# Kernel tuning notes

Hardware: AMD Instinct MI355X
Metric: run time of the kernel (lower is better)

## Reference

```python
import jax, jax.numpy as jnp
import numpy as np

N = 5000          # nodes (pool_ratios = [2000/5000, 0.5])
KS = (2000, 1000, 500)  # top-k sizes per level, depth=3
H = 128           # inter_dim
IN = 3            # xyz
OUT = 6890        # SMPL template vertices
E = 80000


def _gcn(adj, x, W, b):
    # GCNConv: add self-loops (weight 1), symmetric normalization
    n = adj.shape[0]
    A = adj + jnp.eye(n, dtype=adj.dtype)
    dinv = jax.lax.rsqrt(A.sum(axis=1))
    Ahat = dinv[:, None] * A * dinv[None, :]
    return Ahat @ (x @ W) + b


def _augment(adj):
    # GraphUNet.augment_adj: remove self loops, add self loops, A @ A, remove self loops
    n = adj.shape[0]
    eye = jnp.eye(n, dtype=adj.dtype)
    A = adj * (1.0 - eye) + eye
    A2 = A @ A
    return A2 * (1.0 - eye)


def _pool(x, adj, w, k):
    # TopKPooling: score = tanh(x.w / ||w||), keep top-k, scale kept features by score
    score = jnp.tanh((x @ w) / jnp.linalg.norm(w))
    sc, perm = jax.lax.top_k(score, k)
    x = x[perm] * sc[:, None]
    adj = adj[perm][:, perm]
    return x, adj, perm


def reference(pos, edge_index, Wd0, bd0, Wd1, bd1, Wd2, bd2, Wd3, bd3,
              pw0, pw1, pw2, Wu0, bu0, Wu1, bu1, Wu2, bu2,
              W1, b1, W2, b2, W3, b3):
    # eval mode: dropout_adj(p=0.1, training=False) is identity
    adj = jnp.zeros((N, N), pos.dtype).at[edge_index[0], edge_index[1]].add(1.0)

    x = jax.nn.relu(_gcn(adj, pos, Wd0, bd0))
    xs, adjs, perms = [x], [adj], []
    Wds = [(Wd1, bd1), (Wd2, bd2), (Wd3, bd3)]
    pws = [pw0, pw1, pw2]

    adj_cur = adj
    for i in range(3):
        a = _augment(adj_cur)
        x, adj_cur, perm = _pool(x, a, pws[i], KS[i])
        Wi, bi = Wds[i]
        x = jax.nn.relu(_gcn(adj_cur, x, Wi, bi))
        if i < 2:
            xs.append(x)
            adjs.append(adj_cur)
        perms.append(perm)

    Wus = [(Wu0, bu0), (Wu1, bu1), (Wu2, bu2)]
    for i in range(3):
        j = 2 - i
        res = xs[j]
        up = jnp.zeros_like(res).at[perms[j]].set(x)  # unpool: scatter back
        x = res + up                                   # sum_res=True
        Wi, bi = Wus[i]
        x = _gcn(adjs[j], x, Wi, bi)
        if i < 2:
            x = jax.nn.relu(x)

    x = x @ W1 + b1
    x = jax.nn.relu(x) @ W2 + b2
    x = x @ W3 + b3
    return jax.nn.log_softmax(x, axis=1)


def _glorot(k, shape):
    return (jax.random.normal(k, shape) * np.sqrt(2.0 / (shape[0] + shape[1]))).astype(jnp.float32)


def setup_inputs() -> dict:
    key = jax.random.key(0)
    ks = jax.random.split(key, 16)
    inp = {
        'pos': jax.random.normal(ks[0], (N, IN), dtype=jnp.float32),
        'edge_index': jax.random.randint(ks[1], (2, E), 0, N, dtype=jnp.int64),
        'Wd0': _glorot(ks[2], (IN, H)), 'bd0': jnp.zeros((H,), jnp.float32),
        'Wd1': _glorot(ks[3], (H, H)), 'bd1': jnp.zeros((H,), jnp.float32),
        'Wd2': _glorot(ks[4], (H, H)), 'bd2': jnp.zeros((H,), jnp.float32),
        'Wd3': _glorot(ks[5], (H, H)), 'bd3': jnp.zeros((H,), jnp.float32),
        'pw0': jax.random.normal(ks[6], (H,), dtype=jnp.float32) / np.sqrt(H),
        'pw1': jax.random.normal(ks[7], (H,), dtype=jnp.float32) / np.sqrt(H),
        'pw2': jax.random.normal(ks[8], (H,), dtype=jnp.float32) / np.sqrt(H),
        'Wu0': _glorot(ks[9], (H, H)), 'bu0': jnp.zeros((H,), jnp.float32),
        'Wu1': _glorot(ks[10], (H, H)), 'bu1': jnp.zeros((H,), jnp.float32),
        'Wu2': _glorot(ks[11], (H, H)), 'bu2': jnp.zeros((H,), jnp.float32),
        'W1': _glorot(ks[12], (H, H)), 'b1': jnp.zeros((H,), jnp.float32),
        'W2': _glorot(ks[13], (H, H)), 'b2': jnp.zeros((H,), jnp.float32),
        'W3': _glorot(ks[14], (H, OUT)), 'b3': jnp.zeros((OUT,), jnp.float32),
    }
    return inp
```

## Files before the change

### kernel.cpp

```cpp
#include <hip/hip_runtime.h>
#include <cmath>

#define CDIV(a,b) (((a)+(b)-1)/(b))

using u16 = unsigned short;
using short8 = __attribute__((ext_vector_type(8))) short;
using f32x4 = __attribute__((ext_vector_type(4))) float;

__device__ __forceinline__ u16 f2b(float v) {
    union { float f; unsigned u; } x; x.f = v;
    unsigned r = x.u + 0x7fffu + ((x.u >> 16) & 1u);
    return (u16)(r >> 16);
}
__device__ __forceinline__ float b2f(u16 h) {
    union { unsigned u; float f; } x; x.u = ((unsigned)h) << 16;
    return x.f;
}

#if defined(__has_builtin)
#if __has_builtin(__builtin_amdgcn_global_load_lds)
#define HAS_GLL 1
#endif
#endif
#ifndef HAS_GLL
#define HAS_GLL 0
#endif

__device__ __forceinline__ void g2l(const u16* g, uint4* l) {
#if HAS_GLL
    __builtin_amdgcn_global_load_lds((const __attribute__((address_space(1))) void*)g,
                                     (__attribute__((address_space(3))) void*)l, 16, 0, 0);
#else
    *l = *(const uint4*)g;
#endif
}


__global__ void build_adj_k(const int* __restrict__ ei, float* __restrict__ adj, int E, int ld) {
    int e = blockIdx.x * 256 + threadIdx.x;
    if (e < E) {
        int s = ei[e];
        int d = ei[E + e];
        atomicAdd(&adj[(size_t)s * ld + d], 1.0f);
    }
}

__global__ void rowsum_dinv_b_k(const u16* __restrict__ adjb, int ld, int n, float* __restrict__ dinv) {
    int i = blockIdx.x;
    __shared__ float red[256];
    const u16* row = adjb + (size_t)i * ld;
    float s = 0.f;
    for (int j = threadIdx.x; j < n; j += 256) s += b2f(row[j]);
    red[threadIdx.x] = s; __syncthreads();
    for (int w = 128; w > 0; w >>= 1) {
        if (threadIdx.x < w) red[threadIdx.x] += red[threadIdx.x + w];
        __syncthreads();
    }
    if (threadIdx.x == 0) dinv[i] = rsqrtf(red[0] + 1.0f);
}

__global__ void conv0_k(const float* __restrict__ in, u16* __restrict__ outS, u16* __restrict__ outT, int n) {
    __shared__ u16 t[64][65];
    int i0 = blockIdx.y * 64, j0 = blockIdx.x * 64;
    for (int e = threadIdx.x; e < 4096; e += 256) {
        int r = e >> 6, c = e & 63;
        u16 v = f2b(in[(size_t)(i0 + r) * n + j0 + c]);
        outS[(size_t)(i0 + r) * n + j0 + c] = v;
        t[r][c] = v;
    }
    __syncthreads();
    for (int e = threadIdx.x; e < 4096; e += 256) {
        int r = e >> 6, c = e & 63;
        outT[(size_t)(j0 + r) * n + i0 + c] = t[c][r];
    }
}

__global__ void transpose_b_k(const u16* __restrict__ in, u16* __restrict__ out, int n) {
    __shared__ u16 t[64][65];
    int i0 = blockIdx.y * 64, j0 = blockIdx.x * 64;
    for (int e = threadIdx.x; e < 4096; e += 256) {
        int r = e >> 6, c = e & 63;
        t[r][c] = in[(size_t)(i0 + r) * n + j0 + c];
    }
    __syncthreads();
    for (int e = threadIdx.x; e < 4096; e += 256) {
        int r = e >> 6, c = e & 63;
        out[(size_t)(j0 + r) * n + i0 + c] = t[c][r];
    }
}


template<int SA, int SB>
__global__ __launch_bounds__(256) void mm_nt(const u16* __restrict__ A0, const u16* __restrict__ A1,
                                             const u16* __restrict__ B0, const u16* __restrict__ B1,
                                             float* __restrict__ C, const float* __restrict__ cbias,
                                             int M, int N, int lda, int ldb, int ldc,
                                             int kPerZ, int Kpad, size_t cstride) {
    __shared__ uint4 lds_t[(2 + SA + SB) * 512];
    uint4* Ab  = lds_t;
    uint4* A1b = lds_t + (SA ? 512 : 0);
    uint4* Bb  = lds_t + (1 + SA) * 512;
    uint4* B1b = Bb + (SB ? 512 : 0);

    int tid = threadIdx.x;

    int nx = gridDim.x, nxy = nx * gridDim.y;
    int bx = blockIdx.x, by = blockIdx.y;
    if ((nxy & 7) == 0) {
        int flat = by * nx + bx;
        int nf = (flat & 7) * (nxy >> 3) + (flat >> 3);
        bx = nf % nx; by = nf / nx;
    }
    int row0 = by * 128, col0 = bx * 128;

    int kbeg = blockIdx.z * kPerZ;
    int kend = min(kbeg + kPerZ, Kpad);
    C += (size_t)blockIdx.z * cstride;

    int wave = tid >> 6, lane = tid & 63;
    int wr = (wave >> 1) * 64, wc = (wave & 1) * 64;
    int lrow = lane & 15, kg = lane >> 4;

    int tS0 = tid, tS1 = tid + 256;
    int R0 = ((tS0 >> 6) << 4) | (tS0 & 15), kc0 = (tS0 >> 4) & 3;
    int R1 = ((tS1 >> 6) << 4) | (tS1 & 15), kc1 = (tS1 >> 4) & 3;

    const u16* aP0 = A0 + (size_t)(row0 + R0) * lda + kbeg + kc0 * 8;
    const u16* aP1 = A0 + (size_t)(row0 + R1) * lda + kbeg + kc1 * 8;
    const u16* bP0 = B0 + (size_t)(col0 + R0) * ldb + kbeg + kc0 * 8;
    const u16* bP1 = B0 + (size_t)(col0 + R1) * ldb + kbeg + kc1 * 8;
    const u16* a1P0 = SA ? (A1 + (size_t)(row0 + R0) * lda + kbeg + kc0 * 8) : nullptr;
    const u16* a1P1 = SA ? (A1 + (size_t)(row0 + R1) * lda + kbeg + kc1 * 8) : nullptr;
    const u16* b1P0 = SB ? (B1 + (size_t)(col0 + R0) * ldb + kbeg + kc0 * 8) : nullptr;
    const u16* b1P1 = SB ? (B1 + (size_t)(col0 + R1) * ldb + kbeg + kc1 * 8) : nullptr;

    f32x4 acc[4][4] = {};

    for (int k0 = kbeg; k0 < kend; k0 += 32) {
        __syncthreads();
        g2l(aP0, Ab + tS0);
        g2l(aP1, Ab + tS1);
        if constexpr (SA) { g2l(a1P0, A1b + tS0); g2l(a1P1, A1b + tS1); }
        g2l(bP0, Bb + tS0);
        g2l(bP1, Bb + tS1);
        if constexpr (SB) { g2l(b1P0, B1b + tS0); g2l(b1P1, B1b + tS1); }
        __syncthreads();

        const short8* Ap  = (const short8*)Ab;
        const short8* A1p = (const short8*)A1b;
        const short8* Bp  = (const short8*)Bb;
        const short8* B1p = (const short8*)B1b;

        short8 a[4], a1[4], b[4], b1[4];
#pragma unroll
        for (int m = 0; m < 4; ++m) {
            int idx = (((wr >> 4) + m) << 6) | (kg << 4) | lrow;
            a[m] = Ap[idx];
            if constexpr (SA) a1[m] = A1p[idx];
        }
#pragma unroll
        for (int n = 0; n < 4; ++n) {
            int idx = (((wc >> 4) + n) << 6) | (kg << 4) | lrow;
            b[n] = Bp[idx];
            if constexpr (SB) b1[n] = B1p[idx];
        }
#pragma unroll
        for (int m = 0; m < 4; ++m)
#pragma unroll
            for (int n = 0; n < 4; ++n) {
                acc[m][n] = __builtin_amdgcn_mfma_f32_16x16x32_bf16(a[m], b[n], acc[m][n], 0, 0, 0);
                if constexpr (SA) acc[m][n] = __builtin_amdgcn_mfma_f32_16x16x32_bf16(a1[m], b[n], acc[m][n], 0, 0, 0);
                if constexpr (SB) acc[m][n] = __builtin_amdgcn_mfma_f32_16x16x32_bf16(a[m], b1[n], acc[m][n], 0, 0, 0);
            }

        aP0 += 32; aP1 += 32; bP0 += 32; bP1 += 32;
        if constexpr (SA) { a1P0 += 32; a1P1 += 32; }
        if constexpr (SB) { b1P0 += 32; b1P1 += 32; }
    }

#pragma unroll
    for (int m = 0; m < 4; ++m) {
        int rm = row0 + wr + m * 16 + kg * 4;
#pragma unroll
        for (int n = 0; n < 4; ++n) {
            int cc = col0 + wc + n * 16 + lrow;
            if (cc >= N) continue;
            float badd = cbias ? cbias[cc] : 0.f;
#pragma unroll
            for (int i = 0; i < 4; ++i) {
                int r = rm + i;
                if (r < M) C[(size_t)r * ldc + cc] = acc[m][n][i] + badd;
            }
        }
    }
}


__global__ __launch_bounds__(256) void gemm64(const float* __restrict__ A, const float* __restrict__ B,
                                              float* __restrict__ C,
                                              int M, int N, int K, int lda, int ldb, int ldc,
                                              const float* __restrict__ bias, int relu) {
    __shared__ float As[16][65];
    __shared__ float Bs[16][65];
    int tid = threadIdx.x;
    int trow = tid / 16, tcol = tid % 16;
    int row0 = blockIdx.y * 64 + trow * 4;
    int col0 = blockIdx.x * 64 + tcol * 4;
    float acc[4][4] = {};
    int am = tid >> 2;
    int ak = (tid & 3) * 4;
    int bk = tid >> 4;
    int bn = (tid & 15) * 4;
    for (int k0 = 0; k0 < K; k0 += 16) {
        int gm = blockIdx.y * 64 + am;
#pragma unroll
        for (int u = 0; u < 4; ++u) {
            int gk = k0 + ak + u;
            As[ak + u][am] = (gm < M && gk < K) ? A[(size_t)gm * lda + gk] : 0.f;
        }
        int gbk = k0 + bk;
#pragma unroll
        for (int u = 0; u < 4; ++u) {
            int gn = blockIdx.x * 64 + bn + u;
            Bs[bk][bn + u] = (gbk < K && gn < N) ? B[(size_t)gbk * ldb + gn] : 0.f;
        }
        __syncthreads();
#pragma unroll
        for (int kk = 0; kk < 16; ++kk) {
            float a[4], b[4];
#pragma unroll
            for (int i = 0; i < 4; ++i) a[i] = As[kk][trow * 4 + i];
#pragma unroll
            for (int j = 0; j < 4; ++j) b[j] = Bs[kk][tcol * 4 + j];
#pragma unroll
            for (int i = 0; i < 4; ++i)
#pragma unroll
                for (int j = 0; j < 4; ++j) acc[i][j] += a[i] * b[j];
        }
        __syncthreads();
    }
#pragma unroll
    for (int i = 0; i < 4; ++i) {
        int r = row0 + i;
        if (r >= M) continue;
#pragma unroll
        for (int j = 0; j < 4; ++j) {
            int c = col0 + j;
            if (c < N) {
                float v = acc[i][j] + (bias ? bias[c] : 0.f);
                if (relu) v = fmaxf(v, 0.f);
                C[(size_t)r * ldc + c] = v;
            }
        }
    }
}


__global__ void scale_split_k(const float* __restrict__ xw, const float* __restrict__ dinv,
                              u16* __restrict__ zhT, u16* __restrict__ zlT, int M, int ldz) {
    __shared__ float t[32][33];
    int i0 = blockIdx.x * 32, f0 = blockIdx.y * 32;
#pragma unroll
    for (int it = 0; it < 4; ++it) {
        int r = it * 8 + (threadIdx.x >> 5);
        int c = threadIdx.x & 31;
        int i = i0 + r;
        t[r][c] = (i < M) ? dinv[i] * xw[(size_t)i * 128 + f0 + c] : 0.f;
    }
    __syncthreads();
#pragma unroll
    for (int it = 0; it < 4; ++it) {
        int r = it * 8 + (threadIdx.x >> 5);
        int c = threadIdx.x & 31;
        int f = f0 + r, i = i0 + c;
        float v = t[c][r];
        u16 h = f2b(v);
        zhT[(size_t)f * ldz + i] = h;
        zlT[(size_t)f * ldz + i] = f2b(v - b2f(h));
    }
}

__global__ void reduce_gcn_post_k(const float* __restrict__ part, int Z, int Mp,
                                  const float* __restrict__ xw, const float* __restrict__ dinv,
                                  const float* __restrict__ bias, float* __restrict__ y, int relu) {
    int i = blockIdx.x, f = threadIdx.x;
    size_t idx = (size_t)i * 128 + f;
    float s = 0.f;
    for (int z = 0; z < Z; ++z) s += part[(size_t)z * Mp * 128 + idx];
    float di = dinv[i];
    float v = di * s + di * di * xw[idx] + bias[f];
    y[idx] = relu ? fmaxf(v, 0.f) : v;
}


__global__ void score_k(const float* __restrict__ x, const float* __restrict__ pw,
                        float* __restrict__ score) {
    int i = blockIdx.x;
    __shared__ float red[128], red2[128];
    float p = pw[threadIdx.x];
    red[threadIdx.x]  = x[(size_t)i * 128 + threadIdx.x] * p;
    red2[threadIdx.x] = p * p;
    __syncthreads();
    for (int s = 64; s > 0; s >>= 1) {
        if (threadIdx.x < s) { red[threadIdx.x] += red[threadIdx.x + s]; red2[threadIdx.x] += red2[threadIdx.x + s]; }
        __syncthreads();
    }
    if (threadIdx.x == 0) score[i] = tanhf(red[0] / sqrtf(red2[0]));
}

__global__ __launch_bounds__(256) void rank_partial_k(const float* __restrict__ score, int n,
                                                      int* __restrict__ rankpart) {
    __shared__ float s_sh[512];
    int i = blockIdx.x * 256 + threadIdx.x;
    int jbase = blockIdx.y * 512;
    float si = (i < n) ? score[i] : -3.0f;
    for (int t = threadIdx.x; t < 512; t += 256) {
        int j = jbase + t;
        s_sh[t] = (j < n) ? score[j] : -3.0f;
    }
    __syncthreads();
    int cnt = 0;
#pragma unroll 16
    for (int t = 0; t < 512; ++t) {
        float sj = s_sh[t];
        cnt += (sj > si) || (sj == si && (jbase + t) < i);
    }
    if (i < n) rankpart[blockIdx.y * n + i] = cnt;
}

__global__ void scatter_topk_k(const float* __restrict__ score, const int* __restrict__ rankpart,
                               int nsl, int n, int k, int* __restrict__ perm, float* __restrict__ sc) {
    int i = blockIdx.x * 256 + threadIdx.x;
    if (i >= n) return;
    int r = 0;
    for (int s = 0; s < nsl; ++s) r += rankpart[s * n + i];
    if (r < k) { perm[r] = i; sc[r] = score[i]; }
}

__global__ void pool_x_k(float* __restrict__ xo, const float* __restrict__ xi,
                         const int* __restrict__ perm, const float* __restrict__ sc) {
    int a = blockIdx.x, f = threadIdx.x;
    xo[(size_t)a * 128 + f] = xi[(size_t)perm[a] * 128 + f] * sc[a];
}

__global__ void gather2_b_k(const u16* __restrict__ src0, const u16* __restrict__ src1,
                            int ldsrc, const int* __restrict__ perm,
                            u16* __restrict__ dst0, u16* __restrict__ dst1, int width) {
    const u16* src = blockIdx.y ? src1 : src0;
    u16* dst = blockIdx.y ? dst1 : dst0;
    int row = blockIdx.x;
    int p = perm[row];
    const uint4* s4 = (const uint4*)(src + (size_t)p * ldsrc);
    uint4* d4 = (uint4*)(dst + (size_t)row * width);
    int n8 = width >> 3;
    for (int j = threadIdx.x; j < n8; j += 256) d4[j] = s4[j];
    __syncthreads();
    if (threadIdx.x == 0) dst[(size_t)row * width + p] = 0x3F80;
}

__global__ void reduce_pool_k(const float* __restrict__ part, int Z, int k, int Mp, u16* __restrict__ out) {
    int row = blockIdx.x;
    for (int j = threadIdx.x; j < Mp; j += 256) {
        float s = 0.f;
        if (row < k && j < k) {
            for (int z = 0; z < Z; ++z) s += part[(size_t)z * Mp * Mp + (size_t)row * Mp + j];
            if (j == row) s = 0.f;
        }
        out[(size_t)row * Mp + j] = f2b(s);
    }
}

__global__ void scatter_add_k(float* __restrict__ xdst, const int* __restrict__ perm,
                              const float* __restrict__ xsrc) {
    int a = blockIdx.x, f = threadIdx.x;
    xdst[(size_t)perm[a] * 128 + f] += xsrc[(size_t)a * 128 + f];
}


__global__ void split_head_k(const float* __restrict__ x, u16* __restrict__ Ah, u16* __restrict__ Al) {
    int i = blockIdx.x, f = threadIdx.x;
    size_t idx = (size_t)i * 128 + f;
    float v = x[idx];
    u16 h = f2b(v);
    Ah[idx] = h;
    Al[idx] = f2b(v - b2f(h));
}

__global__ void convW3T_k(const float* __restrict__ W3, u16* __restrict__ W3T, int Nc, int Ncp) {
    __shared__ float t[64][65];
    int k0 = blockIdx.y * 64, n0 = blockIdx.x * 64;
    for (int e = threadIdx.x; e < 4096; e += 256) {
        int r = e >> 6, c = e & 63;
        t[r][c] = (k0 + r < 128 && n0 + c < Nc) ? W3[(size_t)(k0 + r) * Nc + n0 + c] : 0.f;
    }
    __syncthreads();
    for (int e = threadIdx.x; e < 4096; e += 256) {
        int r = e >> 6, c = e & 63;
        int nn = n0 + r, kk = k0 + c;
        if (nn < Ncp) W3T[(size_t)nn * 128 + kk] = f2b(t[c][r]);
    }
}

__global__ __launch_bounds__(256) void logsoftmax_k(float* __restrict__ out) {
    const int C = 6890;
    const int CPT = 27;
    int row = blockIdx.x;
    float* rowp = out + (size_t)row * C;
    __shared__ float red[256];

    float v[CPT];
    float mx = -1e30f;
#pragma unroll
    for (int u = 0; u < CPT; ++u) {
        int c = threadIdx.x + u * 256;
        v[u] = (c < C) ? rowp[c] : -1e30f;
        mx = fmaxf(mx, v[u]);
    }
    red[threadIdx.x] = mx; __syncthreads();
    for (int s = 128; s > 0; s >>= 1) {
        if (threadIdx.x < s) red[threadIdx.x] = fmaxf(red[threadIdx.x], red[threadIdx.x + s]);
        __syncthreads();
    }
    float m = red[0];
    __syncthreads();

    float sum = 0.f;
#pragma unroll
    for (int u = 0; u < CPT; ++u) sum += __expf(v[u] - m);
    red[threadIdx.x] = sum; __syncthreads();
    for (int s = 128; s > 0; s >>= 1) {
        if (threadIdx.x < s) red[threadIdx.x] += red[threadIdx.x + s];
        __syncthreads();
    }
    float ls = m + logf(red[0]);

#pragma unroll
    for (int u = 0; u < CPT; ++u) {
        int c = threadIdx.x + u * 256;
        if (c < C) rowp[c] = v[u] - ls;
    }
}


extern "C" void kernel_launch(void* const* d_in, const int* in_sizes, int n_in,
                              void* d_out, int out_size, void* d_ws, size_t ws_size,
                              hipStream_t stream) {
    const int N0 = 5000, K1 = 2000, K2 = 1000, K3 = 500, E = 80000, OUTC = 6890;
    const int Np0 = 5120, Kp1 = 2048, Kp2 = 1024, Kp3 = 512, OUTCP = 6912;
    (void)in_sizes; (void)n_in; (void)out_size; (void)ws_size;

    const float* pos = (const float*)d_in[0];
    const int*   ei  = (const int*)d_in[1];
    const float* Wd0 = (const float*)d_in[2];  const float* bd0 = (const float*)d_in[3];
    const float* Wd1 = (const float*)d_in[4];  const float* bd1 = (const float*)d_in[5];
    const float* Wd2 = (const float*)d_in[6];  const float* bd2 = (const float*)d_in[7];
    const float* Wd3 = (const float*)d_in[8];  const float* bd3 = (const float*)d_in[9];
    const float* pw0 = (const float*)d_in[10];
    const float* pw1 = (const float*)d_in[11];
    const float* pw2 = (const float*)d_in[12];
    const float* Wu0 = (const float*)d_in[13]; const float* bu0 = (const float*)d_in[14];
    const float* Wu1 = (const float*)d_in[15]; const float* bu1 = (const float*)d_in[16];
    const float* Wu2 = (const float*)d_in[17]; const float* bu2 = (const float*)d_in[18];
    const float* W1  = (const float*)d_in[19]; const float* b1  = (const float*)d_in[20];
    const float* W2  = (const float*)d_in[21]; const float* b2  = (const float*)d_in[22];
    const float* W3  = (const float*)d_in[23]; const float* b3  = (const float*)d_in[24];

    float* w = (float*)d_ws;
    size_t off = 0;
    auto alloc = [&](size_t nel) { float* p = w + off; off += nel; return p; };

    float* pool = alloc(26220000);
    float* adj0 = pool;
    float* partials = pool;
    u16* G   = (u16*)(pool + 13000000);
    u16* HT  = (u16*)(pool + 18250000);
    u16* zhT = (u16*)(pool + 13000000);
    u16* zlT = (u16*)(pool + 13400000);
    u16* Ah  = (u16*)(pool);
    u16* Al  = (u16*)(pool + 400000);

    u16* adj0b  = (u16*)alloc(13107200);
    u16* adj0bT = (u16*)alloc(13107200);
    u16* adj1b  = (u16*)alloc(2097152);
    u16* adj1bT = (u16*)alloc(2097152);
    u16* adj2b  = (u16*)alloc(524288);
    u16* adj2bT = (u16*)alloc(524288);
    u16* adj3b  = (u16*)alloc(131072);
    u16* W3T    = (u16*)alloc(442368);

    float* x0 = alloc((size_t)N0 * 128);
    float* x1 = alloc((size_t)K1 * 128);
    float* x2 = alloc((size_t)K2 * 128);
    float* xa = alloc((size_t)N0 * 128);
    float* xb = alloc((size_t)N0 * 128);
    float* xw = alloc((size_t)N0 * 128);
    float* dinv0 = alloc(N0); float* dinv1 = alloc(K1); float* dinv2 = alloc(K2); float* dinv3 = alloc(K3);
    float* scorev = alloc(N0);
    float* scv    = alloc(K1);
    int* perm0 = (int*)alloc(K1);
    int* perm1 = (int*)alloc(K2);
    int* perm2 = (int*)alloc(K3);
    int* rankpart = (int*)alloc(50048);

    auto launch_mm = [&](int SA, int SB, const u16* A0, const u16* A1, const u16* B0, const u16* B1,
                         float* Cc, const float* cbias, int M, int N, int Kpad,
                         int lda, int ldb, int ldc, size_t cstride, int Z) -> int {
        int kPerZ = CDIV(Kpad, Z * 32) * 32;
        int gz = CDIV(Kpad, kPerZ);
        dim3 g(CDIV(N, 128), CDIV(M, 128), gz);
        if (SA)      mm_nt<1, 0><<<g, 256, 0, stream>>>(A0, A1, B0, B1, Cc, cbias, M, N, lda, ldb, ldc, kPerZ, Kpad, cstride);
        else if (SB) mm_nt<0, 1><<<g, 256, 0, stream>>>(A0, A1, B0, B1, Cc, cbias, M, N, lda, ldb, ldc, kPerZ, Kpad, cstride);
        else         mm_nt<0, 0><<<g, 256, 0, stream>>>(A0, A1, B0, B1, Cc, cbias, M, N, lda, ldb, ldc, kPerZ, Kpad, cstride);
        return gz;
    };

    auto run_gcn = [&](const u16* adjb, int n, int Np,
                       const float* x, int kin, const float* W, const float* bias,
                       const float* dinv, int relu, float* y, int Z) {
        gemm64<<<dim3(2, CDIV(n, 64)), 256, 0, stream>>>(x, W, xw, n, 128, kin, kin, 128, 128, nullptr, 0);
        scale_split_k<<<dim3(Np / 32, 4), 256, 0, stream>>>(xw, dinv, zhT, zlT, n, Np);
        int gz = launch_mm(0, 1, adjb, nullptr, zhT, zlT, partials, nullptr,
                           Np, 128, Np, Np, Np, 128, (size_t)Np * 128, Z);
        reduce_gcn_post_k<<<n, 128, 0, stream>>>(partials, gz, Np, xw, dinv, bias, y, relu);
    };

    auto run_pool = [&](const float* x, int n, int Np, int kNew, int KpNew, const float* pw,
                        const u16* srcb, const u16* srcbT, u16* adjNew, int* perm, int Z) {
        score_k<<<n, 128, 0, stream>>>(x, pw, scorev);
        int nsl = CDIV(n, 512);
        rank_partial_k<<<dim3(CDIV(n, 256), nsl), 256, 0, stream>>>(scorev, n, rankpart);
        scatter_topk_k<<<CDIV(n, 256), 256, 0, stream>>>(scorev, rankpart, nsl, n, kNew, perm, scv);
        pool_x_k<<<kNew, 128, 0, stream>>>(xa, x, perm, scv);
        gather2_b_k<<<dim3(kNew, 2), 256, 0, stream>>>(srcb, srcbT, Np, perm, G, HT, Np);
        int gz = launch_mm(0, 0, G, nullptr, HT, nullptr, partials, nullptr,
                           KpNew, KpNew, Np, Np, Np, KpNew, (size_t)KpNew * KpNew, Z);
        reduce_pool_k<<<KpNew, 256, 0, stream>>>(partials, gz, kNew, KpNew, adjNew);
    };

    hipMemsetAsync(adj0, 0, (size_t)Np0 * Np0 * sizeof(float), stream);
    build_adj_k<<<CDIV(E, 256), 256, 0, stream>>>(ei, adj0, E, Np0);
    conv0_k<<<dim3(Np0 / 64, Np0 / 64), 256, 0, stream>>>(adj0, adj0b, adj0bT, Np0);
    rowsum_dinv_b_k<<<N0, 256, 0, stream>>>(adj0b, Np0, Np0, dinv0);

    run_gcn(adj0b, N0, Np0, pos, 3, Wd0, bd0, dinv0, 1, x0, 10);

    run_pool(x0, N0, Np0, K1, Kp1, pw0, adj0b, adj0bT, adj1b, perm0, 3);
    transpose_b_k<<<dim3(Kp1 / 64, Kp1 / 64), 256, 0, stream>>>(adj1b, adj1bT, Kp1);
    rowsum_dinv_b_k<<<K1, 256, 0, stream>>>(adj1b, Kp1, Kp1, dinv1);
    run_gcn(adj1b, K1, Kp1, xa, 128, Wd1, bd1, dinv1, 1, x1, 16);

    run_pool(x1, K1, Kp1, K2, Kp2, pw1, adj1b, adj1bT, adj2b, perm1, 8);
    transpose_b_k<<<dim3(Kp2 / 64, Kp2 / 64), 256, 0, stream>>>(adj2b, adj2bT, Kp2);
    rowsum_dinv_b_k<<<K2, 256, 0, stream>>>(adj2b, Kp2, Kp2, dinv2);
    run_gcn(adj2b, K2, Kp2, xa, 128, Wd2, bd2, dinv2, 1, x2, 16);

    run_pool(x2, K2, Kp2, K3, Kp3, pw2, adj2b, adj2bT, adj3b, perm2, 8);
    rowsum_dinv_b_k<<<K3, 256, 0, stream>>>(adj3b, Kp3, Kp3, dinv3);
    run_gcn(adj3b, K3, Kp3, xa, 128, Wd3, bd3, dinv3, 1, xb, 8);

    hipMemcpyAsync(xa, x2, (size_t)K2 * 128 * sizeof(float), hipMemcpyDeviceToDevice, stream);
    scatter_add_k<<<K3, 128, 0, stream>>>(xa, perm2, xb);
    run_gcn(adj2b, K2, Kp2, xa, 128, Wu0, bu0, dinv2, 1, xb, 16);

    hipMemcpyAsync(xa, x1, (size_t)K1 * 128 * sizeof(float), hipMemcpyDeviceToDevice, stream);
    scatter_add_k<<<K2, 128, 0, stream>>>(xa, perm1, xb);
    run_gcn(adj1b, K1, Kp1, xa, 128, Wu1, bu1, dinv1, 1, xb, 16);

    hipMemcpyAsync(xa, x0, (size_t)N0 * 128 * sizeof(float), hipMemcpyDeviceToDevice, stream);
    scatter_add_k<<<K1, 128, 0, stream>>>(xa, perm0, xb);
    run_gcn(adj0b, N0, Np0, xa, 128, Wu2, bu2, dinv0, 0, xb, 10);

    gemm64<<<dim3(2, CDIV(N0, 64)), 256, 0, stream>>>(xb, W1, xa, N0, 128, 128, 128, 128, 128, b1, 1);
    gemm64<<<dim3(2, CDIV(N0, 64)), 256, 0, stream>>>(xa, W2, xw, N0, 128, 128, 128, 128, 128, b2, 0);

    split_head_k<<<N0, 128, 0, stream>>>(xw, Ah, Al);
    convW3T_k<<<dim3(OUTCP / 64, 2), 256, 0, stream>>>(W3, W3T, OUTC, OUTCP);

    float* outp = (float*)d_out;
    launch_mm(1, 0, Ah, Al, W3T, nullptr, outp, b3, N0, OUTC, 128, 128, 128, OUTC, 0, 1);
    logsoftmax_k<<<N0, 256, 0, stream>>>(outp);
}
```

Measured before the change: 878.0 us.

## Replace first-level dense augment GEMM with sparse CSR SpGEMM on kept rows

```diff
diff --git a/kernel.cpp b/kernel.cpp
--- a/kernel.cpp
+++ b/kernel.cpp
@@ -59,19 +59,13 @@
     if (threadIdx.x == 0) dinv[i] = rsqrtf(red[0] + 1.0f);
 }
 
-__global__ void conv0_k(const float* __restrict__ in, u16* __restrict__ outS, u16* __restrict__ outT, int n) {
-    __shared__ u16 t[64][65];
-    int i0 = blockIdx.y * 64, j0 = blockIdx.x * 64;
-    for (int e = threadIdx.x; e < 4096; e += 256) {
-        int r = e >> 6, c = e & 63;
-        u16 v = f2b(in[(size_t)(i0 + r) * n + j0 + c]);
-        outS[(size_t)(i0 + r) * n + j0 + c] = v;
-        t[r][c] = v;
-    }
-    __syncthreads();
-    for (int e = threadIdx.x; e < 4096; e += 256) {
-        int r = e >> 6, c = e & 63;
-        outT[(size_t)(j0 + r) * n + i0 + c] = t[c][r];
+__global__ void convS_k(const float* __restrict__ in, u16* __restrict__ out, size_t n4) {
+    size_t i = (size_t)blockIdx.x * 256 + threadIdx.x;
+    if (i < n4) {
+        float4 v = ((const float4*)in)[i];
+        ushort4 o;
+        o.x = f2b(v.x); o.y = f2b(v.y); o.z = f2b(v.z); o.w = f2b(v.w);
+        ((ushort4*)out)[i] = o;
     }
 }
 
@@ -86,6 +80,91 @@
     for (int e = threadIdx.x; e < 4096; e += 256) {
         int r = e >> 6, c = e & 63;
         out[(size_t)(j0 + r) * n + i0 + c] = t[c][r];
+    }
+}
+
+
+__global__ void csr_cnt_k(const int* __restrict__ ei, int E, int* __restrict__ rowcnt) {
+    int e = blockIdx.x * 256 + threadIdx.x;
+    if (e < E) {
+        int u = ei[e], v = ei[E + e];
+        if (u != v) atomicAdd(&rowcnt[u], 1);
+    }
+}
+
+__global__ __launch_bounds__(1024) void prefix_k(const int* __restrict__ cnt, int* __restrict__ ptr, int n) {
+    __shared__ int buf[5120];
+    for (int i = threadIdx.x; i < 5120; i += 1024) buf[i] = (i < n) ? cnt[i] : 0;
+    __syncthreads();
+    for (int d = 1; d < 5120; d <<= 1) {
+        int vals[5];
+#pragma unroll
+        for (int c = 0; c < 5; ++c) {
+            int i = threadIdx.x + c * 1024;
+            vals[c] = (i >= d) ? buf[i - d] : 0;
+        }
+        __syncthreads();
+#pragma unroll
+        for (int c = 0; c < 5; ++c) {
+            int i = threadIdx.x + c * 1024;
+            buf[i] += vals[c];
+        }
+        __syncthreads();
+    }
+    for (int i = threadIdx.x; i <= n; i += 1024) ptr[i] = (i == 0) ? 0 : buf[i - 1];
+}
+
+__global__ void csr_fill_k(const int* __restrict__ ei, int E, const int* __restrict__ rowptr,
+                           int* __restrict__ fill, int* __restrict__ cols) {
+    int e = blockIdx.x * 256 + threadIdx.x;
+    if (e < E) {
+        int u = ei[e], v = ei[E + e];
+        if (u != v) {
+            int p = rowptr[u] + atomicAdd(&fill[u], 1);
+            cols[p] = v;
+        }
+    }
+}
+
+__global__ void inv_k(const int* __restrict__ perm, int k, int* __restrict__ inv) {
+    int r = blockIdx.x * 256 + threadIdx.x;
+    if (r < k) inv[perm[r]] = r;
+}
+
+__global__ __launch_bounds__(256) void spgemm_k(const int* __restrict__ perm, const int* __restrict__ rowptr,
+                                                const int* __restrict__ cols, const int* __restrict__ inv,
+                                                int* __restrict__ A2, int ldo) {
+    __shared__ int nb[256];
+    __shared__ int degs;
+    int a = blockIdx.x;
+    int pa = perm[a];
+    int s = rowptr[pa], epos = rowptr[pa + 1];
+    int d = epos - s;
+    if (threadIdx.x == 0) degs = d > 256 ? 256 : d;
+    if (threadIdx.x < d && threadIdx.x < 256) nb[threadIdx.x] = cols[s + threadIdx.x];
+    __syncthreads();
+    int* rowA2 = A2 + (size_t)a * ldo;
+    for (int p = s + threadIdx.x; p < epos; p += 256) {
+        int b = inv[cols[p]];
+        if (b >= 0) atomicAdd(&rowA2[b], 2);
+    }
+    int dd = degs;
+    for (int j = 0; j < dd; ++j) {
+        int kk = nb[j];
+        int s2 = rowptr[kk], e2 = rowptr[kk + 1];
+        for (int p = s2 + threadIdx.x; p < e2; p += 256) {
+            int b = inv[cols[p]];
+            if (b >= 0) atomicAdd(&rowA2[b], 1);
+        }
+    }
+}
+
+__global__ void conv_spg_k(const int* __restrict__ A2, int kNew, int Mp, u16* __restrict__ out) {
+    int r = blockIdx.x;
+    for (int j = threadIdx.x; j < Mp; j += 256) {
+        int v = 0;
+        if (r < kNew && j < kNew && j != r) v = A2[(size_t)r * Mp + j];
+        out[(size_t)r * Mp + j] = f2b((float)v);
     }
 }
 
@@ -480,7 +559,6 @@
     u16* Al  = (u16*)(pool + 400000);
 
     u16* adj0b  = (u16*)alloc(13107200);
-    u16* adj0bT = (u16*)alloc(13107200);
     u16* adj1b  = (u16*)alloc(2097152);
     u16* adj1bT = (u16*)alloc(2097152);
     u16* adj2b  = (u16*)alloc(524288);
@@ -501,6 +579,11 @@
     int* perm1 = (int*)alloc(K2);
     int* perm2 = (int*)alloc(K3);
     int* rankpart = (int*)alloc(50048);
+    int* rowcnt = (int*)alloc(5120);
+    int* rowptr = (int*)alloc(5120);
+    int* fillc  = (int*)alloc(5120);
+    int* colsb  = (int*)alloc(80000);
+    int* invb   = (int*)alloc(5120);
 
     auto launch_mm = [&](int SA, int SB, const u16* A0, const u16* A1, const u16* B0, const u16* B1,
                          float* Cc, const float* cbias, int M, int N, int Kpad,
@@ -538,13 +621,31 @@
     };
 
     hipMemsetAsync(adj0, 0, (size_t)Np0 * Np0 * sizeof(float), stream);
+    hipMemsetAsync(rowcnt, 0, N0 * sizeof(int), stream);
+    hipMemsetAsync(fillc, 0, N0 * sizeof(int), stream);
     build_adj_k<<<CDIV(E, 256), 256, 0, stream>>>(ei, adj0, E, Np0);
-    conv0_k<<<dim3(Np0 / 64, Np0 / 64), 256, 0, stream>>>(adj0, adj0b, adj0bT, Np0);
+    csr_cnt_k<<<CDIV(E, 256), 256, 0, stream>>>(ei, E, rowcnt);
+    prefix_k<<<1, 1024, 0, stream>>>(rowcnt, rowptr, N0);
+    csr_fill_k<<<CDIV(E, 256), 256, 0, stream>>>(ei, E, rowptr, fillc, colsb);
+    convS_k<<<CDIV((size_t)Np0 * Np0 / 4, 256), 256, 0, stream>>>(adj0, adj0b, (size_t)Np0 * Np0 / 4);
     rowsum_dinv_b_k<<<N0, 256, 0, stream>>>(adj0b, Np0, Np0, dinv0);
 
     run_gcn(adj0b, N0, Np0, pos, 3, Wd0, bd0, dinv0, 1, x0, 10);
 
-    run_pool(x0, N0, Np0, K1, Kp1, pw0, adj0b, adj0bT, adj1b, perm0, 3);
+    score_k<<<N0, 128, 0, stream>>>(x0, pw0, scorev);
+    {
+        int nsl = CDIV(N0, 512);
+        rank_partial_k<<<dim3(CDIV(N0, 256), nsl), 256, 0, stream>>>(scorev, N0, rankpart);
+        scatter_topk_k<<<CDIV(N0, 256), 256, 0, stream>>>(scorev, rankpart, nsl, N0, K1, perm0, scv);
+    }
+    pool_x_k<<<K1, 128, 0, stream>>>(xa, x0, perm0, scv);
+    hipMemsetAsync(invb, 0xFF, N0 * sizeof(int), stream);
+    inv_k<<<CDIV(K1, 256), 256, 0, stream>>>(perm0, K1, invb);
+    int* A2i = (int*)partials;
+    hipMemsetAsync(A2i, 0, (size_t)Kp1 * Kp1 * sizeof(int), stream);
+    spgemm_k<<<K1, 256, 0, stream>>>(perm0, rowptr, colsb, invb, A2i, Kp1);
+    conv_spg_k<<<Kp1, 256, 0, stream>>>(A2i, K1, Kp1, adj1b);
+
     transpose_b_k<<<dim3(Kp1 / 64, Kp1 / 64), 256, 0, stream>>>(adj1b, adj1bT, Kp1);
     rowsum_dinv_b_k<<<K1, 256, 0, stream>>>(adj1b, Kp1, Kp1, dinv1);
     run_gcn(adj1b, K1, Kp1, xa, 128, Wd1, bd1, dinv1, 1, x1, 16);
```

Result: faster. 817.1 us (-6.9%).
